# Kernel tuning notes

Measured on AMD Instinct MI355X. Metric: run time of the kernel, lower is better.

Reference implementation:

```python
import jax, jax.numpy as jnp
import numpy as np

N_COMP = 48
RES = 300
N_FEAT = 27
N_PTS = 1_000_000


def _sample_plane(plane, gx, gy):
    # plane: [C, H, W]; gx, gy: [N] grid coords in [-1, 1]; bilinear, align_corners=True
    C, H, W = plane.shape
    x = (gx + 1.0) * 0.5 * (W - 1)
    y = (gy + 1.0) * 0.5 * (H - 1)
    x0f = jnp.floor(x)
    y0f = jnp.floor(y)
    wx = x - x0f
    wy = y - y0f
    x0 = jnp.clip(x0f, 0, W - 1).astype(jnp.int32)
    y0 = jnp.clip(y0f, 0, H - 1).astype(jnp.int32)
    x1 = jnp.clip(x0 + 1, 0, W - 1)
    y1 = jnp.clip(y0 + 1, 0, H - 1)
    v00 = plane[:, y0, x0]  # [C, N]
    v01 = plane[:, y0, x1]
    v10 = plane[:, y1, x0]
    v11 = plane[:, y1, x1]
    return (1.0 - wy) * ((1.0 - wx) * v00 + wx * v01) + wy * ((1.0 - wx) * v10 + wx * v11)


def _sample_line(line, gy):
    # line: [C, R] (width dim of size 1 squeezed; grid x == 0 -> column 0); gy: [N]
    C, R = line.shape
    y = (gy + 1.0) * 0.5 * (R - 1)
    y0f = jnp.floor(y)
    wy = y - y0f
    y0 = jnp.clip(y0f, 0, R - 1).astype(jnp.int32)
    y1 = jnp.clip(y0 + 1, 0, R - 1)
    return (1.0 - wy) * line[:, y0] + wy * line[:, y1]  # [C, N]


def setup_inputs():
    key = jax.random.key(0)
    k0, k1, k2, k3 = jax.random.split(key, 4)
    xyz = jax.random.uniform(k0, (N_PTS, 3), jnp.float32) * 2.0 - 1.0
    planes = 0.1 * jax.random.uniform(k1, (3, N_COMP, RES, RES), jnp.float32)
    lines = 0.1 * jax.random.uniform(k2, (3, N_COMP, RES, 1), jnp.float32)
    basis_W = jax.random.normal(k3, (N_FEAT, 3 * N_COMP), jnp.float32) / jnp.sqrt(3.0 * N_COMP)
    return {"xyz_sampled": xyz, "planes": planes, "lines": lines, "basis_W": basis_W}


def reference(xyz_sampled, planes, lines, basis_W):
    # plane i samples (x=xyz[:,a], y=xyz[:,b]) with (a,b) per torch's xyz[..., [2,1]/[2,0]/[1,0]]
    PLANE_AX = ((2, 1), (2, 0), (1, 0))
    pf, lf = [], []
    for i in range(3):
        a, b = PLANE_AX[i]
        pf.append(_sample_plane(planes[i], xyz_sampled[:, a], xyz_sampled[:, b]))
        lf.append(_sample_line(lines[i, :, :, 0], xyz_sampled[:, i]))
    pf = jnp.concatenate(pf, axis=0)  # [3C, N]
    lf = jnp.concatenate(lf, axis=0)  # [3C, N]
    # basis_mat: Linear(3C -> n_features, bias=False) applied to (pf*lf).T
    return (pf * lf).T @ basis_W.T  # [N, n_features]
```

## Files before the change

### kernel.cpp

```cpp
#include <hip/hip_runtime.h>

namespace {

constexpr int NCOMP = 48;
constexpr int RESN  = 300;
constexpr int NFEAT = 27;
constexpr int NPTS  = 1000000;
constexpr int CCTOT = 3 * NCOMP;
constexpr int GRID1 = 32;
constexpr int NBUCKET = GRID1 * GRID1 * GRID1;

typedef _Float16 half_t;
typedef __attribute__((ext_vector_type(8))) _Float16 half8;
typedef __attribute__((ext_vector_type(8))) short          short8;
typedef __attribute__((ext_vector_type(8))) unsigned short ushort8;
typedef __attribute__((ext_vector_type(4))) float          floatx4;

__device__ __forceinline__ unsigned short f32_to_bf16(float x) {
    unsigned u = __float_as_uint(x);
    u += 0x7fffu + ((u >> 16) & 1u);
    return (unsigned short)(u >> 16);
}

constexpr int SH_STRIDE = 56;

constexpr int TP_TOTAL  = 3 * RESN * RESN;
constexpr int TP_BLOCKS = (TP_TOTAL + 255) / 256;
constexpr int LINES_TOT = 3 * RESN;
constexpr int WT_TOT    = NFEAT * CCTOT;
constexpr int WFRAG_TOT = 3 * 2 * 2 * 64 * 8;
constexpr int SU_TOTAL  = LINES_TOT + WT_TOT + WFRAG_TOT;
constexpr int SU_BLOCKS = (SU_TOTAL + 255) / 256;
constexpr int HB_BLOCKS = (NPTS + 255) / 256;

__device__ __forceinline__ int cell_of(float q) {
    float t = (q + 1.0f) * (0.5f * (float)GRID1);
    int c = (int)t;
    return min(max(c, 0), GRID1 - 1);
}
__device__ __forceinline__ int key_of(float q0, float q1, float q2) {
    return (cell_of(q0) * GRID1 + cell_of(q1)) * GRID1 + cell_of(q2);
}

__global__ __launch_bounds__(256) void fused_front_k(
    const float* __restrict__ planes, const float* __restrict__ lines,
    const float* __restrict__ W, const float* __restrict__ xyz,
    half_t* __restrict__ pt, half_t* __restrict__ lt,
    float* __restrict__ wt, unsigned short* __restrict__ wfrag,
    int* __restrict__ hist) {
    int b = blockIdx.x;
    if (b < TP_BLOCKS) {
        int idx = b * 256 + threadIdx.x;
        if (idx >= TP_TOTAL) return;
        int i   = idx / (RESN * RESN);
        int rem = idx - i * (RESN * RESN);
        const float* s = planes + (size_t)i * NCOMP * RESN * RESN + rem;
        half8* d = (half8*)(pt + (size_t)idx * NCOMP);
#pragma unroll
        for (int g = 0; g < NCOMP / 8; ++g) {
            half8 h;
#pragma unroll
            for (int k = 0; k < 8; ++k)
                h[k] = (half_t)s[(size_t)(g * 8 + k) * (RESN * RESN)];
            d[g] = h;
        }
        return;
    }
    if (b < TP_BLOCKS + SU_BLOCKS) {
        int idx = (b - TP_BLOCKS) * 256 + threadIdx.x;
        if (idx < LINES_TOT) {
            int i = idx / RESN;
            int y = idx - i * RESN;
            const float* s = lines + (size_t)i * NCOMP * RESN + y;
            half8* d = (half8*)(lt + (size_t)idx * NCOMP);
#pragma unroll
            for (int g = 0; g < NCOMP / 8; ++g) {
                half8 h;
#pragma unroll
                for (int k = 0; k < 8; ++k)
                    h[k] = (half_t)s[(size_t)(g * 8 + k) * RESN];
                d[g] = h;
            }
            return;
        }
        idx -= LINES_TOT;
        if (idx < WT_TOT) {
            int f  = idx / CCTOT;
            int cc = idx - f * CCTOT;
            wt[(size_t)cc * NFEAT + f] = W[idx];
            return;
        }
        idx -= WT_TOT;
        if (idx < WFRAG_TOT) {
            int j    = idx & 7;
            int lane = (idx >> 3) & 63;
            int nn   = (idx >> 9) & 1;
            int kb   = (idx >> 10) & 1;
            int md   = idx >> 11;
            int f  = nn * 16 + (lane & 15);
            int kk = kb * 32 + ((lane >> 4) << 3) + j;
            float vf = 0.0f;
            if (f < NFEAT && kk < NCOMP)
                vf = W[(size_t)f * CCTOT + md * NCOMP + kk];
            wfrag[idx] = f32_to_bf16(vf);
        }
        return;
    }
    int p = (b - TP_BLOCKS - SU_BLOCKS) * 256 + threadIdx.x;
    if (p >= NPTS || !hist) return;
    float q0 = xyz[3 * (size_t)p + 0];
    float q1 = xyz[3 * (size_t)p + 1];
    float q2 = xyz[3 * (size_t)p + 2];
    atomicAdd(&hist[key_of(q0, q1, q2)], 1);
}


__global__ __launch_bounds__(1024) void scan_k(const int* __restrict__ hist,
                                               int* __restrict__ start) {
    __shared__ int part[1024];
    int t = threadIdx.x;
    int base = t * (NBUCKET / 1024);
    int s = 0;
#pragma unroll 4
    for (int j = 0; j < NBUCKET / 1024; ++j) s += hist[base + j];
    part[t] = s;
    __syncthreads();
    for (int off = 1; off < 1024; off <<= 1) {
        int v = (t >= off) ? part[t - off] : 0;
        __syncthreads();
        part[t] += v;
        __syncthreads();
    }
    int run = (t == 0) ? 0 : part[t - 1];
    for (int j = 0; j < NBUCKET / 1024; ++j) {
        start[base + j] = run;
        run += hist[base + j];
    }
}

__global__ __launch_bounds__(256) void scatter_k(const float* __restrict__ xyz,
                                                 int* __restrict__ start,
                                                 float4* __restrict__ xyzs) {
    int p = blockIdx.x * blockDim.x + threadIdx.x;
    if (p >= NPTS) return;
    float q0 = xyz[3 * (size_t)p + 0];
    float q1 = xyz[3 * (size_t)p + 1];
    float q2 = xyz[3 * (size_t)p + 2];
    int slot = atomicAdd(&start[key_of(q0, q1, q2)], 1);
    float4 v;
    v.x = q0; v.y = q1; v.z = q2; v.w = __int_as_float(p);
    xyzs[slot] = v;
}


__device__ __forceinline__ void produce_mode(float gx, float gy, float gl,
                                             const half_t* __restrict__ pt_i,
                                             const half_t* __restrict__ lt_i,
                                             unsigned short* __restrict__ shrow) {
    float x = (gx + 1.0f) * 0.5f * (float)(RESN - 1);
    float y = (gy + 1.0f) * 0.5f * (float)(RESN - 1);
    float l = (gl + 1.0f) * 0.5f * (float)(RESN - 1);
    float x0f = floorf(x), y0f = floorf(y), l0f = floorf(l);
    float wx = x - x0f, wy = y - y0f, wl = l - l0f;
    int x0 = max(0, min((int)x0f, RESN - 1));
    int y0 = max(0, min((int)y0f, RESN - 1));
    int l0 = max(0, min((int)l0f, RESN - 1));
    int x1 = min(x0 + 1, RESN - 1);
    int y1 = min(y0 + 1, RESN - 1);
    int l1 = min(l0 + 1, RESN - 1);
    float w00 = (1.0f - wy) * (1.0f - wx);
    float w01 = (1.0f - wy) * wx;
    float w10 = wy * (1.0f - wx);
    float w11 = wy * wx;
    float wl0 = 1.0f - wl;
    float wl1 = wl;

    const half8* p00 = (const half8*)(pt_i + ((size_t)y0 * RESN + x0) * NCOMP);
    const half8* p01 = (const half8*)(pt_i + ((size_t)y0 * RESN + x1) * NCOMP);
    const half8* p10 = (const half8*)(pt_i + ((size_t)y1 * RESN + x0) * NCOMP);
    const half8* p11 = (const half8*)(pt_i + ((size_t)y1 * RESN + x1) * NCOMP);
    const half8* L0  = (const half8*)(lt_i + (size_t)l0 * NCOMP);
    const half8* L1  = (const half8*)(lt_i + (size_t)l1 * NCOMP);

#pragma unroll 2
    for (int g = 0; g < NCOMP / 8; ++g) {
        half8 a = p00[g], b = p01[g], c = p10[g], d = p11[g];
        half8 e0 = L0[g], e1 = L1[g];
        ushort8 h;
#pragma unroll
        for (int j = 0; j < 8; ++j) {
            float pv = w00 * (float)a[j] + w01 * (float)b[j]
                     + w10 * (float)c[j] + w11 * (float)d[j];
            float lv = wl0 * (float)e0[j] + wl1 * (float)e1[j];
            h[j] = f32_to_bf16(pv * lv);
        }
        *(ushort8*)(shrow + g * 8) = h;
    }
}

__device__ __forceinline__ void mfma_phase(const unsigned short* __restrict__ shw,
                                           int r, int q,
                                           short8 blo0, short8 blo1,
                                           short8 bhi0, short8 bhi1,
                                           floatx4 acc[4][2]) {
    const short8 z8 = {0, 0, 0, 0, 0, 0, 0, 0};
#pragma unroll
    for (int m = 0; m < 4; ++m) {
        const unsigned short* rb = shw + (size_t)(m * 16 + r) * SH_STRIDE;
        short8 alo = *(const short8*)(rb + q * 8);
        short8 ahl = *(const short8*)(rb + 32 + (q & 1) * 8);
        short8 ahi = (q < 2) ? ahl : z8;
        acc[m][0] = __builtin_amdgcn_mfma_f32_16x16x32_bf16(alo, blo0, acc[m][0], 0, 0, 0);
        acc[m][0] = __builtin_amdgcn_mfma_f32_16x16x32_bf16(ahi, bhi0, acc[m][0], 0, 0, 0);
        acc[m][1] = __builtin_amdgcn_mfma_f32_16x16x32_bf16(alo, blo1, acc[m][1], 0, 0, 0);
        acc[m][1] = __builtin_amdgcn_mfma_f32_16x16x32_bf16(ahi, bhi1, acc[m][1], 0, 0, 0);
    }
}

constexpr int MAIN_BLK = 128;
constexpr int MAIN_NWG = (NPTS + MAIN_BLK - 1) / MAIN_BLK;

__device__ __forceinline__ int swz_main(int orig) {
    constexpr int Q = MAIN_NWG / 8, R = MAIN_NWG % 8;
    int x = orig & 7, p = orig >> 3;
    return (x < R ? x * (Q + 1) : R * (Q + 1) + (x - R) * Q) + p;
}

__global__ __launch_bounds__(MAIN_BLK) void tensor_vm_mfma_kernel(
    const float4* __restrict__ xyzs,
    const half_t* __restrict__ pt,
    const half_t* __restrict__ lt,
    const unsigned short* __restrict__ wfrag,
    float* __restrict__ out) {
    __shared__ unsigned short sh[2][64][SH_STRIDE];

    const int bid = swz_main(blockIdx.x);
    const int tid = threadIdx.x;
    const int w  = tid >> 6;
    const int ln = tid & 63;
    const int r  = ln & 15;
    const int q  = ln >> 4;
    const int gidx = bid * MAIN_BLK + tid;
    const int i = min(gidx, NPTS - 1);
    float4 v = xyzs[i];
    const float q0 = v.x, q1 = v.y, q2 = v.z;
    const int permInt = __float_as_int(v.w);

    floatx4 acc[4][2];
    const floatx4 z = {0.f, 0.f, 0.f, 0.f};
#pragma unroll
    for (int m = 0; m < 4; ++m) { acc[m][0] = z; acc[m][1] = z; }

    constexpr size_t PSZ = (size_t)RESN * RESN * NCOMP;
    constexpr size_t LSZ = (size_t)RESN * NCOMP;

    unsigned short* shrow = &sh[w][ln][0];
    const unsigned short* shw = &sh[w][0][0];

    const float gxs[3] = {q2, q2, q1};
    const float gys[3] = {q1, q0, q0};
    const float gls[3] = {q0, q1, q2};

#pragma unroll
    for (int md = 0; md < 3; ++md) {
        const unsigned short* wfb = wfrag + (size_t)md * 2048 + (size_t)ln * 8;
        short8 blo0 = *(const short8*)(wfb);
        short8 blo1 = *(const short8*)(wfb + 512);
        short8 bhi0 = *(const short8*)(wfb + 1024);
        short8 bhi1 = *(const short8*)(wfb + 1536);

        produce_mode(gxs[md], gys[md], gls[md], pt + md * PSZ, lt + md * LSZ, shrow);
        asm volatile("s_waitcnt lgkmcnt(0)" ::: "memory");
        __builtin_amdgcn_sched_barrier(0);
        mfma_phase(shw, r, q, blo0, blo1, bhi0, bhi1, acc);
        __builtin_amdgcn_sched_barrier(0);
    }

    const int blockBase = bid * MAIN_BLK + w * 64;
#pragma unroll
    for (int m = 0; m < 4; ++m) {
#pragma unroll
        for (int rr = 0; rr < 4; ++rr) {
            const int pl = m * 16 + q * 4 + rr;
            const int pp = __shfl(permInt, pl);
            if (blockBase + pl < NPTS) {
                float* o = out + (size_t)pp * NFEAT + r;
                o[0] = acc[m][0][rr];
                if (r < NFEAT - 16) o[16] = acc[m][1][rr];
            }
        }
    }
}


__device__ __forceinline__ void accum_mode(float gx, float gy, float gl,
                                           const half_t* __restrict__ pt_i,
                                           const half_t* __restrict__ lt_i,
                                           const float* __restrict__ wt_i,
                                           float* __restrict__ acc) {
    float x = (gx + 1.0f) * 0.5f * (float)(RESN - 1);
    float y = (gy + 1.0f) * 0.5f * (float)(RESN - 1);
    float l = (gl + 1.0f) * 0.5f * (float)(RESN - 1);
    float x0f = floorf(x), y0f = floorf(y), l0f = floorf(l);
    float wx = x - x0f, wy = y - y0f, wl = l - l0f;
    int x0 = (int)x0f; x0 = max(0, min(x0, RESN - 1));
    int y0 = (int)y0f; y0 = max(0, min(y0, RESN - 1));
    int l0 = (int)l0f; l0 = max(0, min(l0, RESN - 1));
    int x1 = min(x0 + 1, RESN - 1);
    int y1 = min(y0 + 1, RESN - 1);
    int l1 = min(l0 + 1, RESN - 1);
    float w00 = (1.0f - wy) * (1.0f - wx);
    float w01 = (1.0f - wy) * wx;
    float w10 = wy * (1.0f - wx);
    float w11 = wy * wx;
    float wl0 = 1.0f - wl;
    float wl1 = wl;
    const half8* p00 = (const half8*)(pt_i + ((size_t)y0 * RESN + x0) * NCOMP);
    const half8* p01 = (const half8*)(pt_i + ((size_t)y0 * RESN + x1) * NCOMP);
    const half8* p10 = (const half8*)(pt_i + ((size_t)y1 * RESN + x0) * NCOMP);
    const half8* p11 = (const half8*)(pt_i + ((size_t)y1 * RESN + x1) * NCOMP);
    const half8* L0  = (const half8*)(lt_i + (size_t)l0 * NCOMP);
    const half8* L1  = (const half8*)(lt_i + (size_t)l1 * NCOMP);
#pragma unroll 2
    for (int g = 0; g < NCOMP / 8; ++g) {
        half8 a = p00[g], b = p01[g], c = p10[g], d = p11[g];
        half8 e0 = L0[g], e1 = L1[g];
#pragma unroll
        for (int j = 0; j < 8; ++j) {
            float pv = w00 * (float)a[j] + w01 * (float)b[j]
                     + w10 * (float)c[j] + w11 * (float)d[j];
            float lv = wl0 * (float)e0[j] + wl1 * (float)e1[j];
            float pr = pv * lv;
            const float* wrow = wt_i + (size_t)(8 * g + j) * NFEAT;
#pragma unroll
            for (int f = 0; f < NFEAT; ++f)
                acc[f] += pr * wrow[f];
        }
    }
}

__global__ __launch_bounds__(256) void tensor_vm_kernel(
    const float* __restrict__ xyz,
    const half_t* __restrict__ pt,
    const half_t* __restrict__ lt,
    const float* __restrict__ wt,
    float* __restrict__ out) {
    int p = blockIdx.x * blockDim.x + threadIdx.x;
    if (p >= NPTS) return;
    float q0 = xyz[3 * (size_t)p + 0];
    float q1 = xyz[3 * (size_t)p + 1];
    float q2 = xyz[3 * (size_t)p + 2];
    float acc[NFEAT];
#pragma unroll
    for (int f = 0; f < NFEAT; ++f) acc[f] = 0.0f;
    constexpr size_t PSZ = (size_t)RESN * RESN * NCOMP;
    constexpr size_t LSZ = (size_t)RESN * NCOMP;
    constexpr int    WSZ = NCOMP * NFEAT;
    accum_mode(q2, q1, q0, pt,           lt,           wt,           acc);
    accum_mode(q2, q0, q1, pt + PSZ,     lt + LSZ,     wt + WSZ,     acc);
    accum_mode(q1, q0, q2, pt + 2 * PSZ, lt + 2 * LSZ, wt + 2 * WSZ, acc);
    float* o = out + (size_t)p * NFEAT;
#pragma unroll
    for (int f = 0; f < NFEAT; ++f) o[f] = acc[f];
}

__global__ __launch_bounds__(256) void tensor_vm_naive_kernel(
    const float* __restrict__ xyz,
    const float* __restrict__ planes,
    const float* __restrict__ lines,
    const float* __restrict__ W,
    float* __restrict__ out) {
    int p = blockIdx.x * blockDim.x + threadIdx.x;
    if (p >= NPTS) return;
    float q[3];
    q[0] = xyz[3 * (size_t)p + 0];
    q[1] = xyz[3 * (size_t)p + 1];
    q[2] = xyz[3 * (size_t)p + 2];
    float acc[NFEAT];
    for (int f = 0; f < NFEAT; ++f) acc[f] = 0.0f;
    const int AX[3] = {2, 2, 1};
    const int BX[3] = {1, 0, 0};
    for (int i = 0; i < 3; ++i) {
        float gx = q[AX[i]], gy = q[BX[i]], gl = q[i];
        float x = (gx + 1.0f) * 0.5f * (float)(RESN - 1);
        float y = (gy + 1.0f) * 0.5f * (float)(RESN - 1);
        float l = (gl + 1.0f) * 0.5f * (float)(RESN - 1);
        float x0f = floorf(x), y0f = floorf(y), l0f = floorf(l);
        float wx = x - x0f, wy = y - y0f, wl = l - l0f;
        int x0 = max(0, min((int)x0f, RESN - 1));
        int y0 = max(0, min((int)y0f, RESN - 1));
        int l0 = max(0, min((int)l0f, RESN - 1));
        int x1 = min(x0 + 1, RESN - 1);
        int y1 = min(y0 + 1, RESN - 1);
        int l1 = min(l0 + 1, RESN - 1);
        float w00 = (1.0f - wy) * (1.0f - wx);
        float w01 = (1.0f - wy) * wx;
        float w10 = wy * (1.0f - wx);
        float w11 = wy * wx;
        const float* pl = planes + (size_t)i * NCOMP * RESN * RESN;
        const float* ln = lines + (size_t)i * NCOMP * RESN;
        for (int c = 0; c < NCOMP; ++c) {
            const float* plc = pl + (size_t)c * RESN * RESN;
            float v00 = plc[(size_t)y0 * RESN + x0];
            float v01 = plc[(size_t)y0 * RESN + x1];
            float v10 = plc[(size_t)y1 * RESN + x0];
            float v11 = plc[(size_t)y1 * RESN + x1];
            float pv = w00 * v00 + w01 * v01 + w10 * v10 + w11 * v11;
            float lv = (1.0f - wl) * ln[(size_t)c * RESN + l0] + wl * ln[(size_t)c * RESN + l1];
            float pr = pv * lv;
            int cc = i * NCOMP + c;
            for (int f = 0; f < NFEAT; ++f)
                acc[f] += pr * W[(size_t)f * CCTOT + cc];
        }
    }
    float* o = out + (size_t)p * NFEAT;
    for (int f = 0; f < NFEAT; ++f) o[f] = acc[f];
}

}

extern "C" void kernel_launch(void* const* d_in, const int* in_sizes, int n_in,
                              void* d_out, int out_size, void* d_ws, size_t ws_size,
                              hipStream_t stream) {
    (void)in_sizes; (void)n_in; (void)out_size;
    const float* xyz    = (const float*)d_in[0];
    const float* planes = (const float*)d_in[1];
    const float* lines  = (const float*)d_in[2];
    const float* W      = (const float*)d_in[3];
    float* out = (float*)d_out;

    constexpr size_t PT_HALVES   = (size_t)3 * RESN * RESN * NCOMP;
    constexpr size_t LT_HALVES   = (size_t)3 * RESN * NCOMP;
    constexpr size_t WT_FLOATS   = (size_t)CCTOT * NFEAT;

    constexpr size_t WT_BYTES    = WT_FLOATS * sizeof(float);
    constexpr size_t WFRAG_BYTES = (size_t)WFRAG_TOT * 2;
    constexpr size_t PT_BYTES    = PT_HALVES * sizeof(half_t);
    constexpr size_t LT_BYTES    = LT_HALVES * sizeof(half_t);
    constexpr size_t HIST_BYTES  = (size_t)NBUCKET * sizeof(int);
    constexpr size_t XYZS_BYTES  = (size_t)NPTS * sizeof(float4);
    constexpr size_t NEED_PLAIN  = WT_BYTES + WFRAG_BYTES + PT_BYTES + LT_BYTES;
    constexpr size_t NEED_SORT   = NEED_PLAIN + 2 * HIST_BYTES + XYZS_BYTES;

    if (ws_size >= NEED_PLAIN) {
        float*          wt    = (float*)d_ws;
        unsigned short* wfrag = (unsigned short*)((char*)d_ws + WT_BYTES);
        half_t*         pt    = (half_t*)((char*)d_ws + WT_BYTES + WFRAG_BYTES);
        half_t*         lt    = (half_t*)((char*)d_ws + WT_BYTES + WFRAG_BYTES + PT_BYTES);
        if (ws_size >= NEED_SORT) {
            int*    hist  = (int*)((char*)d_ws + NEED_PLAIN);
            int*    start = (int*)((char*)d_ws + NEED_PLAIN + HIST_BYTES);
            float4* xyzs  = (float4*)((char*)d_ws + NEED_PLAIN + 2 * HIST_BYTES);
            hipMemsetAsync(hist, 0, HIST_BYTES, stream);
            fused_front_k<<<TP_BLOCKS + SU_BLOCKS + HB_BLOCKS, 256, 0, stream>>>(
                planes, lines, W, xyz, pt, lt, wt, wfrag, hist);
            scan_k<<<1, 1024, 0, stream>>>(hist, start);
            scatter_k<<<(NPTS + 255) / 256, 256, 0, stream>>>(xyz, start, xyzs);
            tensor_vm_mfma_kernel<<<MAIN_NWG, MAIN_BLK, 0, stream>>>(
                xyzs, pt, lt, wfrag, out);
        } else {
            fused_front_k<<<TP_BLOCKS + SU_BLOCKS, 256, 0, stream>>>(
                planes, lines, W, xyz, pt, lt, wt, wfrag, nullptr);
            tensor_vm_kernel<<<(NPTS + 255) / 256, 256, 0, stream>>>(xyz, pt, lt, wt, out);
        }
    } else {
        tensor_vm_naive_kernel<<<(NPTS + 255) / 256, 256, 0, stream>>>(xyz, planes, lines, W, out);
    }
}
```

Baseline: 446.4 us.

## Redistribute plane/line gathers across lanes via LDS-staged per-point sample params

Each lane now computes bilinear offsets and weights for its own point and stages them in shared memory. The wave then loops over (point, 8-channel group) pairs, so neighbouring lanes fetch contiguous 16-byte chunks of the same texel instead of each lane striding through 96-byte rows alone. x1/l1 are now always taken as the next texel (+96 bytes) without clamping, which relies on zero weights at edges and on a zero pad added after the line table. Launch bounds also request 4 blocks per CU.

Measured after the change: 402.4 us. -9.9%, faster.

```diff
diff --git a/kernel.cpp b/kernel.cpp
--- a/kernel.cpp
+++ b/kernel.cpp
@@ -24,12 +24,14 @@
 
 constexpr int SH_STRIDE = 56;
 
+constexpr int LT_PAD = 64;
+
 constexpr int TP_TOTAL  = 3 * RESN * RESN;
 constexpr int TP_BLOCKS = (TP_TOTAL + 255) / 256;
 constexpr int LINES_TOT = 3 * RESN;
 constexpr int WT_TOT    = NFEAT * CCTOT;
 constexpr int WFRAG_TOT = 3 * 2 * 2 * 64 * 8;
-constexpr int SU_TOTAL  = LINES_TOT + WT_TOT + WFRAG_TOT;
+constexpr int SU_TOTAL  = LINES_TOT + WT_TOT + WFRAG_TOT + LT_PAD;
 constexpr int SU_BLOCKS = (SU_TOTAL + 255) / 256;
 constexpr int HB_BLOCKS = (NPTS + 255) / 256;
 
@@ -103,7 +105,10 @@
             if (f < NFEAT && kk < NCOMP)
                 vf = W[(size_t)f * CCTOT + md * NCOMP + kk];
             wfrag[idx] = f32_to_bf16(vf);
-        }
+            return;
+        }
+        idx -= WFRAG_TOT;
+        if (idx < LT_PAD) lt[(size_t)3 * RESN * NCOMP + idx] = (half_t)0.f;
         return;
     }
     int p = (b - TP_BLOCKS - SU_BLOCKS) * 256 + threadIdx.x;
@@ -153,51 +158,6 @@
 }
 
 
-__device__ __forceinline__ void produce_mode(float gx, float gy, float gl,
-                                             const half_t* __restrict__ pt_i,
-                                             const half_t* __restrict__ lt_i,
-                                             unsigned short* __restrict__ shrow) {
-    float x = (gx + 1.0f) * 0.5f * (float)(RESN - 1);
-    float y = (gy + 1.0f) * 0.5f * (float)(RESN - 1);
-    float l = (gl + 1.0f) * 0.5f * (float)(RESN - 1);
-    float x0f = floorf(x), y0f = floorf(y), l0f = floorf(l);
-    float wx = x - x0f, wy = y - y0f, wl = l - l0f;
-    int x0 = max(0, min((int)x0f, RESN - 1));
-    int y0 = max(0, min((int)y0f, RESN - 1));
-    int l0 = max(0, min((int)l0f, RESN - 1));
-    int x1 = min(x0 + 1, RESN - 1);
-    int y1 = min(y0 + 1, RESN - 1);
-    int l1 = min(l0 + 1, RESN - 1);
-    float w00 = (1.0f - wy) * (1.0f - wx);
-    float w01 = (1.0f - wy) * wx;
-    float w10 = wy * (1.0f - wx);
-    float w11 = wy * wx;
-    float wl0 = 1.0f - wl;
-    float wl1 = wl;
-
-    const half8* p00 = (const half8*)(pt_i + ((size_t)y0 * RESN + x0) * NCOMP);
-    const half8* p01 = (const half8*)(pt_i + ((size_t)y0 * RESN + x1) * NCOMP);
-    const half8* p10 = (const half8*)(pt_i + ((size_t)y1 * RESN + x0) * NCOMP);
-    const half8* p11 = (const half8*)(pt_i + ((size_t)y1 * RESN + x1) * NCOMP);
-    const half8* L0  = (const half8*)(lt_i + (size_t)l0 * NCOMP);
-    const half8* L1  = (const half8*)(lt_i + (size_t)l1 * NCOMP);
-
-#pragma unroll 2
-    for (int g = 0; g < NCOMP / 8; ++g) {
-        half8 a = p00[g], b = p01[g], c = p10[g], d = p11[g];
-        half8 e0 = L0[g], e1 = L1[g];
-        ushort8 h;
-#pragma unroll
-        for (int j = 0; j < 8; ++j) {
-            float pv = w00 * (float)a[j] + w01 * (float)b[j]
-                     + w10 * (float)c[j] + w11 * (float)d[j];
-            float lv = wl0 * (float)e0[j] + wl1 * (float)e1[j];
-            h[j] = f32_to_bf16(pv * lv);
-        }
-        *(ushort8*)(shrow + g * 8) = h;
-    }
-}
-
 __device__ __forceinline__ void mfma_phase(const unsigned short* __restrict__ shw,
                                            int r, int q,
                                            short8 blo0, short8 blo1,
@@ -226,13 +186,14 @@
     return (x < R ? x * (Q + 1) : R * (Q + 1) + (x - R) * Q) + p;
 }
 
-__global__ __launch_bounds__(MAIN_BLK) void tensor_vm_mfma_kernel(
+__global__ __launch_bounds__(MAIN_BLK, 4) void tensor_vm_mfma_kernel(
     const float4* __restrict__ xyzs,
     const half_t* __restrict__ pt,
     const half_t* __restrict__ lt,
     const unsigned short* __restrict__ wfrag,
     float* __restrict__ out) {
     __shared__ unsigned short sh[2][64][SH_STRIDE];
+    __shared__ float          sp[2][64][8];
 
     const int bid = swz_main(blockIdx.x);
     const int tid = threadIdx.x;
@@ -243,7 +204,6 @@
     const int gidx = bid * MAIN_BLK + tid;
     const int i = min(gidx, NPTS - 1);
     float4 v = xyzs[i];
-    const float q0 = v.x, q1 = v.y, q2 = v.z;
     const int permInt = __float_as_int(v.w);
 
     floatx4 acc[4][2];
@@ -254,12 +214,11 @@
     constexpr size_t PSZ = (size_t)RESN * RESN * NCOMP;
     constexpr size_t LSZ = (size_t)RESN * NCOMP;
 
-    unsigned short* shrow = &sh[w][ln][0];
     const unsigned short* shw = &sh[w][0][0];
 
-    const float gxs[3] = {q2, q2, q1};
-    const float gys[3] = {q1, q0, q0};
-    const float gls[3] = {q0, q1, q2};
+    const float gxs[3] = {v.z, v.z, v.y};
+    const float gys[3] = {v.y, v.x, v.x};
+    const float gls[3] = {v.x, v.y, v.z};
 
 #pragma unroll
     for (int md = 0; md < 3; ++md) {
@@ -269,7 +228,61 @@
         short8 bhi0 = *(const short8*)(wfb + 1024);
         short8 bhi1 = *(const short8*)(wfb + 1536);
 
-        produce_mode(gxs[md], gys[md], gls[md], pt + md * PSZ, lt + md * LSZ, shrow);
+        {
+            float x = (gxs[md] + 1.0f) * 0.5f * (float)(RESN - 1);
+            float y = (gys[md] + 1.0f) * 0.5f * (float)(RESN - 1);
+            float l = (gls[md] + 1.0f) * 0.5f * (float)(RESN - 1);
+            float x0f = floorf(x), y0f = floorf(y), l0f = floorf(l);
+            float wx = x - x0f, wy = y - y0f, wl = l - l0f;
+            int x0 = max(0, min((int)x0f, RESN - 1));
+            int y0 = max(0, min((int)y0f, RESN - 1));
+            int l0 = max(0, min((int)l0f, RESN - 1));
+            int y1 = min(y0 + 1, RESN - 1);
+            int off0 = (y0 * RESN + x0) * NCOMP * 2;
+            int off1 = (y1 * RESN + x0) * NCOMP * 2;
+            int offL = l0 * NCOMP * 2;
+            float4 A, B;
+            A.x = __int_as_float(off0); A.y = __int_as_float(off1);
+            A.z = __int_as_float(offL); A.w = (1.0f - wy) * (1.0f - wx);
+            B.x = (1.0f - wy) * wx; B.y = wy * (1.0f - wx);
+            B.z = wy * wx;          B.w = wl;
+            *(float4*)&sp[w][ln][0] = A;
+            *(float4*)&sp[w][ln][4] = B;
+        }
+        __builtin_amdgcn_sched_barrier(0);
+
+        const char* pmd = (const char*)(pt + md * PSZ);
+        const char* lmd = (const char*)(lt + md * LSZ);
+#pragma unroll
+        for (int it = 0; it < 6; ++it) {
+            unsigned pair = (unsigned)(it * 64 + ln);
+            unsigned p = (pair * 10923u) >> 16;
+            unsigned s = pair - p * 6u;
+            float4 A = *(const float4*)&sp[w][p][0];
+            float4 B = *(const float4*)&sp[w][p][4];
+            int off0 = __float_as_int(A.x);
+            int off1 = __float_as_int(A.y);
+            int offL = __float_as_int(A.z);
+            float w00 = A.w, w01 = B.x, w10 = B.y, w11 = B.z, wl = B.w;
+            int so = (int)(s * 16u);
+            half8 a = *(const half8*)(pmd + off0 + so);
+            half8 b = *(const half8*)(pmd + off0 + 96 + so);
+            half8 c = *(const half8*)(pmd + off1 + so);
+            half8 d = *(const half8*)(pmd + off1 + 96 + so);
+            half8 e = *(const half8*)(lmd + offL + so);
+            half8 f = *(const half8*)(lmd + offL + 96 + so);
+            float wl0 = 1.0f - wl;
+            ushort8 h;
+#pragma unroll
+            for (int j = 0; j < 8; ++j) {
+                float pv = w00 * (float)a[j] + w01 * (float)b[j]
+                         + w10 * (float)c[j] + w11 * (float)d[j];
+                float lv = wl0 * (float)e[j] + wl * (float)f[j];
+                h[j] = f32_to_bf16(pv * lv);
+            }
+            *(ushort8*)(&sh[w][p][s * 8u]) = h;
+        }
+
         asm volatile("s_waitcnt lgkmcnt(0)" ::: "memory");
         __builtin_amdgcn_sched_barrier(0);
         mfma_phase(shw, r, q, blo0, blo1, bhi0, bhi1, acc);
@@ -430,7 +443,7 @@
     float* out = (float*)d_out;
 
     constexpr size_t PT_HALVES   = (size_t)3 * RESN * RESN * NCOMP;
-    constexpr size_t LT_HALVES   = (size_t)3 * RESN * NCOMP;
+    constexpr size_t LT_HALVES   = (size_t)3 * RESN * NCOMP + LT_PAD;
     constexpr size_t WT_FLOATS   = (size_t)CCTOT * NFEAT;
 
     constexpr size_t WT_BYTES    = WT_FLOATS * sizeof(float);
```
